# Optimization experiments

Hardware: AMD Instinct MI355X
Metric: run time of the kernel (lower is better)

## Reference

```python
import jax, jax.numpy as jnp
import numpy as np

MARGIN = 0.25
GAMMA = 256.0
NEG_INF = -1e30


def setup_inputs() -> dict:
    key = jax.random.key(0)
    k1, k2 = jax.random.split(key)
    B, D = 8192, 128
    return {
        "embeddings_a": jax.random.normal(k1, (B, D), dtype=jnp.float32),
        "embeddings_b": jax.random.normal(k2, (B, D), dtype=jnp.float32),
    }


def _l2_normalize(x, eps=1e-12):
    # matches F.normalize(p=2, dim=1): x / max(||x||, eps)
    n = jnp.sqrt(jnp.sum(x * x, axis=1, keepdims=True))
    return x / jnp.maximum(n, eps)


def reference(embeddings_a, embeddings_b):
    B = embeddings_a.shape[0]
    a = _l2_normalize(embeddings_a)
    b = _l2_normalize(embeddings_b)
    sim = a @ b.T  # [B, B]

    pos_mask = jnp.eye(B, dtype=bool)  # labels=None path

    # positive logits: -gamma * relu((1-m) - s) * (s - m)
    logit_pos = -GAMMA * jnp.maximum((1.0 - MARGIN) - sim, 0.0) * (sim - MARGIN)
    # negative logits:  gamma * relu(s - m) * (s + m)
    logit_neg = GAMMA * jnp.maximum(sim - MARGIN, 0.0) * (sim + MARGIN)

    # masked per-row logsumexp over positive / negative sets
    lse_pos = jax.nn.logsumexp(jnp.where(pos_mask, logit_pos, NEG_INF), axis=1)
    lse_neg = jax.nn.logsumexp(jnp.where(pos_mask, NEG_INF, logit_neg), axis=1)

    losses = jax.nn.softplus(lse_pos + lse_neg)  # [B]
    return jnp.mean(losses)  # reduction='mean'
```

## Files before the change

kernel.cpp:

```cpp
#include <hip/hip_runtime.h>


#define B_N 8192
#define D_K 128
#define MARGIN 0.25f
#define M2 (MARGIN * MARGIN)
#define GAMMA 256.0f

#define BM 128
#define BN 128
#define NCH 8
#define CPB (B_N / NCH)
#define NSUB (CPB / BN)

typedef __attribute__((ext_vector_type(8))) short short8;
typedef __attribute__((ext_vector_type(4))) float f32x4;

__device__ __forceinline__ unsigned short f2bf(float x) {
  unsigned u = __float_as_uint(x);
  u += 0x7FFFu + ((u >> 16) & 1u);
  return (unsigned short)(u >> 16);
}

__device__ __forceinline__ void gload_lds16(const void* gsrc, void* ldst) {
  __builtin_amdgcn_global_load_lds(
      (const __attribute__((address_space(1))) void*)gsrc,
      (__attribute__((address_space(3))) void*)ldst, 16, 0, 0);
}

__global__ __launch_bounds__(256) void norm_diag_kernel(
    const float* __restrict__ a, const float* __restrict__ b,
    unsigned short* __restrict__ abf, unsigned short* __restrict__ bbf,
    float* __restrict__ diag) {
  int wave = threadIdx.x >> 6, lane = threadIdx.x & 63;
  int r = blockIdx.x * 4 + wave;
  int half = lane >> 5, l32 = lane & 31;
  const float* src = half ? b : a;
  unsigned short* dst = half ? bbf : abf;

  float4 v = ((const float4*)(src + (size_t)r * D_K))[l32];
  float ss = v.x * v.x + v.y * v.y + v.z * v.z + v.w * v.w;
  #pragma unroll
  for (int m = 16; m >= 1; m >>= 1) ss += __shfl_xor(ss, m);
  float inv = 1.0f / fmaxf(sqrtf(ss), 1e-12f);
  float n0 = v.x * inv, n1 = v.y * inv, n2 = v.z * inv, n3 = v.w * inv;

  ushort4 o = {f2bf(n0), f2bf(n1), f2bf(n2), f2bf(n3)};
  ((ushort4*)(dst + (size_t)r * D_K))[l32] = o;

  float d = n0 * __shfl_xor(n0, 32) + n1 * __shfl_xor(n1, 32) +
            n2 * __shfl_xor(n2, 32) + n3 * __shfl_xor(n3, 32);
  #pragma unroll
  for (int m = 16; m >= 1; m >>= 1) d += __shfl_xor(d, m);
  if (lane == 0) diag[r] = d;
}

__global__ __launch_bounds__(256, 2) void simlse_kernel(
    const unsigned short* __restrict__ abf, const unsigned short* __restrict__ bbf,
    float* __restrict__ partS) {
  __shared__ __align__(16) unsigned short L[2][BM * D_K];
  __shared__ float sred[BM][2];

  const int tid = threadIdx.x;
  const int wave = tid >> 6, lane = tid & 63;
  const int r16 = lane & 15, kq = lane >> 4;
  const int wr = wave >> 1, wc = wave & 1;
  const int rowBase = blockIdx.y * BM;
  const int chunk = blockIdx.x;

  #pragma unroll
  for (int it = 0; it < 8; ++it) {
    int gb = it * 256 + wave * 64;
    int g = gb + lane;
    int row = g >> 4, sl = g & 15;
    int sls = sl ^ (row & 7);
    gload_lds16(abf + (size_t)(rowBase + row) * D_K + sls * 8, &L[0][gb * 8]);
  }
  {
    const int colBase = chunk * CPB;
    #pragma unroll
    for (int it = 0; it < 8; ++it) {
      int gb = it * 256 + wave * 64;
      int g = gb + lane;
      int row = g >> 4, sl = g & 15;
      int sls = sl ^ (row & 7);
      gload_lds16(bbf + (size_t)(colBase + row) * D_K + sls * 8, &L[1][gb * 8]);
    }
  }
  __syncthreads();

  short8 af[4][4];
  #pragma unroll
  for (int mi = 0; mi < 4; ++mi) {
    int row = wr * 64 + mi * 16 + r16;
    #pragma unroll
    for (int ks = 0; ks < 4; ++ks) {
      int slot = (ks * 4 + kq) ^ (row & 7);
      af[mi][ks] = *(const short8*)&L[0][row * D_K + slot * 8];
    }
  }
  __syncthreads();

  {
    const int colBase = chunk * CPB + BN;
    #pragma unroll
    for (int it = 0; it < 8; ++it) {
      int gb = it * 256 + wave * 64;
      int g = gb + lane;
      int row = g >> 4, sl = g & 15;
      int sls = sl ^ (row & 7);
      gload_lds16(bbf + (size_t)(colBase + row) * D_K + sls * 8, &L[0][gb * 8]);
    }
  }

  float Ssum[4][4];
  #pragma unroll
  for (int mi = 0; mi < 4; ++mi)
    #pragma unroll
    for (int r = 0; r < 4; ++r) Ssum[mi][r] = 0.0f;

  #pragma unroll 2
  for (int st = 0; st < NSUB; ++st) {
    const unsigned short* cb = L[(st + 1) & 1];

    f32x4 acc[4][4];
    const f32x4 z4 = {0.f, 0.f, 0.f, 0.f};
    #pragma unroll
    for (int mi = 0; mi < 4; ++mi)
      #pragma unroll
      for (int ni = 0; ni < 4; ++ni) acc[mi][ni] = z4;

    #pragma unroll
    for (int ks = 0; ks < 4; ++ks) {
      short8 bf[4];
      #pragma unroll
      for (int ni = 0; ni < 4; ++ni) {
        int row = wc * 64 + ni * 16 + r16;
        int slot = (ks * 4 + kq) ^ (row & 7);
        bf[ni] = *(const short8*)&cb[row * D_K + slot * 8];
      }
      #pragma unroll
      for (int mi = 0; mi < 4; ++mi)
        #pragma unroll
        for (int ni = 0; ni < 4; ++ni)
          acc[mi][ni] = __builtin_amdgcn_mfma_f32_16x16x32_bf16(
              af[mi][ks], bf[ni], acc[mi][ni], 0, 0, 0);
    }

    #pragma unroll
    for (int mi = 0; mi < 4; ++mi)
      #pragma unroll
      for (int ni = 0; ni < 4; ++ni) {
        f32x4 v = acc[mi][ni];
        float mx = fmaxf(fmaxf(v[0], v[1]), fmaxf(v[2], v[3]));
        if (__any(mx > MARGIN)) {
          #pragma unroll
          for (int r = 0; r < 4; ++r) {
            float s = v[r];
            float t = fmaf(s, s, -M2);
            float z = (s > MARGIN) ? GAMMA * t : 0.0f;
            Ssum[mi][r] += __expf(z) - 1.0f;
          }
        }
      }

    __syncthreads();

    if (st + 2 < NSUB) {
      const int colBase = chunk * CPB + (st + 2) * BN;
      #pragma unroll
      for (int it = 0; it < 8; ++it) {
        int gb = it * 256 + wave * 64;
        int g = gb + lane;
        int row = g >> 4, sl = g & 15;
        int sls = sl ^ (row & 7);
        gload_lds16(bbf + (size_t)(colBase + row) * D_K + sls * 8,
                    &((unsigned short*)L[(st + 1) & 1])[gb * 8]);
      }
    }
  }

  #pragma unroll
  for (int mi = 0; mi < 4; ++mi)
    #pragma unroll
    for (int r = 0; r < 4; ++r) {
      float v = Ssum[mi][r];
      v += __shfl_xor(v, 1);
      v += __shfl_xor(v, 2);
      v += __shfl_xor(v, 4);
      v += __shfl_xor(v, 8);
      if (r16 == 0) sred[wr * 64 + mi * 16 + kq * 4 + r][wc] = v;
    }
  __syncthreads();
  if (tid < BM)
    partS[(size_t)chunk * B_N + rowBase + tid] = sred[tid][0] + sred[tid][1];
}

__global__ __launch_bounds__(256) void rowfin_kernel(
    const float* __restrict__ partS, const float* __restrict__ diag,
    float* __restrict__ bpart) {
  __shared__ float red[256];
  int i = blockIdx.x * 256 + threadIdx.x;
  float S = 0.0f;
  #pragma unroll
  for (int c = 0; c < NCH; ++c) S += partS[(size_t)c * B_N + i];
  float sd = diag[i];
  float td = fmaf(sd, sd, -M2);
  float zd = (sd > MARGIN) ? GAMMA * td : 0.0f;
  float ed = __expf(zd);
  float lneg = __logf((float)B_N + S - ed);
  float lpos = -GAMMA * fmaxf((1.0f - MARGIN) - sd, 0.0f) * (sd - MARGIN);
  float x = lpos + lneg;
  float loss = fmaxf(x, 0.0f) + log1pf(__expf(-fabsf(x)));
  red[threadIdx.x] = loss;
  __syncthreads();
  #pragma unroll
  for (int s = 128; s >= 1; s >>= 1) {
    if (threadIdx.x < s) red[threadIdx.x] += red[threadIdx.x + s];
    __syncthreads();
  }
  if (threadIdx.x == 0) bpart[blockIdx.x] = red[0];
}

__global__ __launch_bounds__(64) void mean_kernel(
    const float* __restrict__ bpart, float* __restrict__ out) {
  int lane = threadIdx.x;
  float v = (lane < 32) ? bpart[lane] : 0.0f;
  #pragma unroll
  for (int m = 32; m >= 1; m >>= 1) v += __shfl_xor(v, m);
  if (lane == 0) out[0] = v * (1.0f / B_N);
}

extern "C" void kernel_launch(void* const* d_in, const int* in_sizes, int n_in,
                              void* d_out, int out_size, void* d_ws, size_t ws_size,
                              hipStream_t stream) {
  const float* a = (const float*)d_in[0];
  const float* b = (const float*)d_in[1];
  float* out = (float*)d_out;

  char* w = (char*)d_ws;
  unsigned short* abf = (unsigned short*)w;
  unsigned short* bbf = (unsigned short*)(w + (size_t)B_N * D_K * 2);
  float* partS = (float*)(w + (size_t)B_N * D_K * 4);
  float* diag = partS + (size_t)NCH * B_N;
  float* bpart = diag + B_N;

  norm_diag_kernel<<<B_N / 4, 256, 0, stream>>>(a, b, abf, bbf, diag);
  simlse_kernel<<<dim3(NCH, B_N / BM), 256, 0, stream>>>(abf, bbf, partS);
  rowfin_kernel<<<B_N / 256, 256, 0, stream>>>(partS, diag, bpart);
  mean_kernel<<<1, 64, 0, stream>>>(bpart, out);
}
```

Before: 41.23 us.

## Double row tile to 256 with 512-thread blocks sharing B tiles

The similarity kernel now processes 256 rows per block with 8 waves, and both row halves share each streamed 128-column B tile in LDS. This halves the global/L2 traffic for B and the number of blocks, with the A tile staged through the same double buffer. The cost is a shift from 512 four-wave blocks to 256 eight-wave blocks, which changes scheduling granularity and LDS pressure. Separately, the row-finalize reduction uses wave shuffles instead of a shared-memory tree with repeated barriers.

```diff
diff --git a/kernel.cpp b/kernel.cpp
--- a/kernel.cpp
+++ b/kernel.cpp
@@ -7,11 +7,12 @@
 #define M2 (MARGIN * MARGIN)
 #define GAMMA 256.0f
 
-#define BM 128
+#define BM 256
 #define BN 128
 #define NCH 8
 #define CPB (B_N / NCH)
 #define NSUB (CPB / BN)
+#define NROWBLK 32
 
 typedef __attribute__((ext_vector_type(8))) short short8;
 typedef __attribute__((ext_vector_type(4))) float f32x4;
@@ -55,10 +56,10 @@
   if (lane == 0) diag[r] = d;
 }
 
-__global__ __launch_bounds__(256, 2) void simlse_kernel(
+__global__ __launch_bounds__(512, 2) void simlse_kernel(
     const unsigned short* __restrict__ abf, const unsigned short* __restrict__ bbf,
     float* __restrict__ partS) {
-  __shared__ __align__(16) unsigned short L[2][BM * D_K];
+  __shared__ __align__(16) unsigned short BB[2][BN * D_K];
   __shared__ float sred[BM][2];
 
   const int tid = threadIdx.x;
@@ -69,49 +70,48 @@
   const int chunk = blockIdx.x;
 
   #pragma unroll
-  for (int it = 0; it < 8; ++it) {
-    int gb = it * 256 + wave * 64;
-    int g = gb + lane;
-    int row = g >> 4, sl = g & 15;
-    int sls = sl ^ (row & 7);
-    gload_lds16(abf + (size_t)(rowBase + row) * D_K + sls * 8, &L[0][gb * 8]);
-  }
-  {
-    const int colBase = chunk * CPB;
-    #pragma unroll
-    for (int it = 0; it < 8; ++it) {
-      int gb = it * 256 + wave * 64;
+  for (int half = 0; half < 2; ++half) {
+    const unsigned short* srcA = abf + (size_t)(rowBase + half * 128) * D_K;
+    #pragma unroll
+    for (int it = 0; it < 4; ++it) {
+      int gb = it * 512 + wave * 64;
       int g = gb + lane;
       int row = g >> 4, sl = g & 15;
       int sls = sl ^ (row & 7);
-      gload_lds16(bbf + (size_t)(colBase + row) * D_K + sls * 8, &L[1][gb * 8]);
+      gload_lds16(srcA + (size_t)row * D_K + sls * 8, &BB[half][gb * 8]);
     }
   }
   __syncthreads();
 
   short8 af[4][4];
-  #pragma unroll
-  for (int mi = 0; mi < 4; ++mi) {
-    int row = wr * 64 + mi * 16 + r16;
-    #pragma unroll
-    for (int ks = 0; ks < 4; ++ks) {
-      int slot = (ks * 4 + kq) ^ (row & 7);
-      af[mi][ks] = *(const short8*)&L[0][row * D_K + slot * 8];
-    }
-  }
-  __syncthreads();
-
   {
-    const int colBase = chunk * CPB + BN;
-    #pragma unroll
-    for (int it = 0; it < 8; ++it) {
-      int gb = it * 256 + wave * 64;
+    const unsigned short* Abuf = BB[wr >> 1];
+    const int rbase = (wr & 1) * 64;
+    #pragma unroll
+    for (int mi = 0; mi < 4; ++mi) {
+      int row = rbase + mi * 16 + r16;
+      #pragma unroll
+      for (int ks = 0; ks < 4; ++ks) {
+        int slot = (ks * 4 + kq) ^ (row & 7);
+        af[mi][ks] = *(const short8*)&Abuf[row * D_K + slot * 8];
+      }
+    }
+  }
+  __syncthreads();
+
+  #pragma unroll
+  for (int h = 0; h < 2; ++h) {
+    const unsigned short* srcB = bbf + (size_t)(chunk * CPB + h * BN) * D_K;
+    #pragma unroll
+    for (int it = 0; it < 4; ++it) {
+      int gb = it * 512 + wave * 64;
       int g = gb + lane;
       int row = g >> 4, sl = g & 15;
       int sls = sl ^ (row & 7);
-      gload_lds16(bbf + (size_t)(colBase + row) * D_K + sls * 8, &L[0][gb * 8]);
-    }
-  }
+      gload_lds16(srcB + (size_t)row * D_K + sls * 8, &BB[h][gb * 8]);
+    }
+  }
+  __syncthreads();
 
   float Ssum[4][4];
   #pragma unroll
@@ -121,7 +121,7 @@
 
   #pragma unroll 2
   for (int st = 0; st < NSUB; ++st) {
-    const unsigned short* cb = L[(st + 1) & 1];
+    const unsigned short* cb = BB[st & 1];
 
     f32x4 acc[4][4];
     const f32x4 z4 = {0.f, 0.f, 0.f, 0.f};
@@ -167,15 +167,16 @@
     __syncthreads();
 
     if (st + 2 < NSUB) {
-      const int colBase = chunk * CPB + (st + 2) * BN;
-      #pragma unroll
-      for (int it = 0; it < 8; ++it) {
-        int gb = it * 256 + wave * 64;
+      const unsigned short* srcB =
+          bbf + (size_t)(chunk * CPB + (st + 2) * BN) * D_K;
+      unsigned short* dstB = (unsigned short*)BB[st & 1];
+      #pragma unroll
+      for (int it = 0; it < 4; ++it) {
+        int gb = it * 512 + wave * 64;
         int g = gb + lane;
         int row = g >> 4, sl = g & 15;
         int sls = sl ^ (row & 7);
-        gload_lds16(bbf + (size_t)(colBase + row) * D_K + sls * 8,
-                    &((unsigned short*)L[(st + 1) & 1])[gb * 8]);
+        gload_lds16(srcB + (size_t)row * D_K + sls * 8, &dstB[gb * 8]);
       }
     }
   }
@@ -199,27 +200,24 @@
 __global__ __launch_bounds__(256) void rowfin_kernel(
     const float* __restrict__ partS, const float* __restrict__ diag,
     float* __restrict__ bpart) {
-  __shared__ float red[256];
-  int i = blockIdx.x * 256 + threadIdx.x;
+  __shared__ float red[4];
+  int tid = threadIdx.x, lane = tid & 63, wid = tid >> 6;
+  int i = blockIdx.x * 256 + tid;
   float S = 0.0f;
   #pragma unroll
   for (int c = 0; c < NCH; ++c) S += partS[(size_t)c * B_N + i];
   float sd = diag[i];
-  float td = fmaf(sd, sd, -M2);
-  float zd = (sd > MARGIN) ? GAMMA * td : 0.0f;
+  float zd = (sd > MARGIN) ? GAMMA * fmaf(sd, sd, -M2) : 0.0f;
   float ed = __expf(zd);
   float lneg = __logf((float)B_N + S - ed);
   float lpos = -GAMMA * fmaxf((1.0f - MARGIN) - sd, 0.0f) * (sd - MARGIN);
   float x = lpos + lneg;
-  float loss = fmaxf(x, 0.0f) + log1pf(__expf(-fabsf(x)));
-  red[threadIdx.x] = loss;
-  __syncthreads();
-  #pragma unroll
-  for (int s = 128; s >= 1; s >>= 1) {
-    if (threadIdx.x < s) red[threadIdx.x] += red[threadIdx.x + s];
-    __syncthreads();
-  }
-  if (threadIdx.x == 0) bpart[blockIdx.x] = red[0];
+  float acc = fmaxf(x, 0.0f) + log1pf(__expf(-fabsf(x)));
+  #pragma unroll
+  for (int m = 32; m >= 1; m >>= 1) acc += __shfl_xor(acc, m);
+  if (lane == 0) red[wid] = acc;
+  __syncthreads();
+  if (tid == 0) bpart[blockIdx.x] = red[0] + red[1] + red[2] + red[3];
 }
 
 __global__ __launch_bounds__(64) void mean_kernel(
@@ -246,7 +244,7 @@
   float* bpart = diag + B_N;
 
   norm_diag_kernel<<<B_N / 4, 256, 0, stream>>>(a, b, abf, bbf, diag);
-  simlse_kernel<<<dim3(NCH, B_N / BM), 256, 0, stream>>>(abf, bbf, partS);
-  rowfin_kernel<<<B_N / 256, 256, 0, stream>>>(partS, diag, bpart);
+  simlse_kernel<<<dim3(NCH, B_N / BM), 512, 0, stream>>>(abf, bbf, partS);
+  rowfin_kernel<<<NROWBLK, 256, 0, stream>>>(partS, diag, bpart);
   mean_kernel<<<1, 64, 0, stream>>>(bpart, out);
 }
```

Measured after the change: 41.44 us. About the same (+0.5%).
